# Performance work log

Hardware: AMD Instinct MI355X
Metric: run time of the kernel (lower is better)

## Reference

```python
import jax, jax.numpy as jnp
import numpy as np

B, C, H, W = 4, 128, 128, 128
NUM_OP = 6
LANG_DIM = 256
NHIDDEN = 128
EPS = 1e-5


def setup_inputs() -> dict:
    key = jax.random.key(0)
    ks = jax.random.split(key, 11)
    s = 0.02
    return {
        "x": jax.random.normal(ks[0], (B, C, H, W), jnp.float32),
        "lang_embed": jax.random.normal(ks[1], (B, LANG_DIM), jnp.float32),
        "input_semantics": jax.random.uniform(ks[2], (B, NUM_OP + 2, H, W), jnp.float32),
        # mlp_shared: Linear(lang_dim -> nhidden)
        "Ws": jax.random.normal(ks[3], (NHIDDEN, LANG_DIM), jnp.float32) * s,
        "bs": jnp.zeros((NHIDDEN,), jnp.float32),
        # mlp_gamma / mlp_beta: Linear(nhidden -> num_op)
        "Wg": jax.random.normal(ks[4], (NUM_OP, NHIDDEN), jnp.float32) * s,
        "bg": jnp.zeros((NUM_OP,), jnp.float32),
        "Wb": jax.random.normal(ks[5], (NUM_OP, NHIDDEN), jnp.float32) * s,
        "bb": jnp.zeros((NUM_OP,), jnp.float32),
        # reduce_dim: Linear(num_op -> 1)
        "Wr": jax.random.normal(ks[6], (1, NUM_OP), jnp.float32) * s,
        "br": jnp.zeros((1,), jnp.float32),
    }


def reference(x, lang_embed, input_semantics, Ws, bs, Wg, bg, Wb, bb, Wr, br):
    # InstanceNorm2d(affine=False): computed by the torch module but its result
    # is UNUSED in the num_op>1 branch (dead code in the original; jit will DCE it).
    mean = jnp.mean(x, axis=(2, 3), keepdims=True)
    var = jnp.var(x, axis=(2, 3), keepdims=True)  # biased variance
    _normalized = (x - mean) * jax.lax.rsqrt(var + EPS)

    # Small MLPs on the language embedding (no nonlinearity in the original).
    actv = lang_embed @ Ws.T + bs            # (b, nhidden)
    gamma = actv @ Wg.T + bg                 # (b, num_op)
    beta = actv @ Wb.T + bb                  # (b, num_op)

    sem = jnp.transpose(input_semantics[:, 2:, :, :], (0, 2, 3, 1))  # (b,h,w,num_op)
    g = gamma[:, None, None, :] * sem        # (b,h,w,num_op)
    be = beta[:, None, None, :] * sem        # (b,h,w,num_op)

    # Torch builds out5d = x[...,None]*(1+g)[:,None] + be[:,None]  (b,c,h,w,num_op)
    # then reduce_dim(out5d).squeeze(). Since Linear(num_op->1) is linear, fuse:
    # out = x * (sum_k wr_k + g @ wr) + be @ wr + br  -- identical math, no 5D buffer.
    wr = Wr[0]                               # (num_op,)
    scale = jnp.sum(wr) + jnp.einsum('bhwk,k->bhw', g, wr)   # (b,h,w)
    shift = jnp.einsum('bhwk,k->bhw', be, wr) + br[0]        # (b,h,w)
    out = x * scale[:, None, :, :] + shift[:, None, :, :]    # (b,c,h,w)
    return out
```

## Files before the change

### kernel.cpp

```cpp
#include <hip/hip_runtime.h>

#define HW 16384
#define NCH 128
#define CCH 8
#define LANG 256
#define NH 128
#define NOP 6

typedef float f4 __attribute__((ext_vector_type(4)));

__global__ __launch_bounds__(256) void coef_kernel(
    const float* __restrict__ lang, const float* __restrict__ Ws,
    const float* __restrict__ bs, const float* __restrict__ Wg,
    const float* __restrict__ bg, const float* __restrict__ Wb,
    const float* __restrict__ bb, const float* __restrict__ Wr,
    const float* __restrict__ br, float* __restrict__ coefs) {
  const int b = blockIdx.x;
  const int tid = threadIdx.x;
  const int wave = tid >> 6, lane = tid & 63;
  __shared__ float actv[NH];

  const f4 lv = *(const f4*)(lang + b * LANG + lane * 4);

  #pragma unroll 8
  for (int m = 0; m < 32; ++m) {
    const int j = wave * 32 + m;
    const f4 wv = *(const f4*)(Ws + (size_t)j * LANG + lane * 4);
    float p = lv.x * wv.x + lv.y * wv.y + lv.z * wv.z + lv.w * wv.w;
    #pragma unroll
    for (int off = 32; off; off >>= 1) p += __shfl_xor(p, off);
    if (lane == 0) actv[j] = p + bs[j];
  }
  __syncthreads();

  const float a0 = actv[lane * 2], a1 = actv[lane * 2 + 1];
  #pragma unroll
  for (int r = 0; r < 3; ++r) {
    const int k = wave + 4 * r;
    const int kk = (k < NOP) ? k : k - NOP;
    const float* W = ((k < NOP) ? Wg : Wb) + kk * NH;
    float p = a0 * W[lane * 2] + a1 * W[lane * 2 + 1];
    #pragma unroll
    for (int off = 32; off; off >>= 1) p += __shfl_xor(p, off);
    if (lane == 0) {
      const float bias = (k < NOP) ? bg[kk] : bb[kk];
      coefs[b * 12 + k] = (p + bias) * Wr[kk];
    }
  }
  if (b == 0 && tid == 0) {
    float s = 0.f;
    #pragma unroll
    for (int k = 0; k < NOP; ++k) s += Wr[k];
    coefs[48] = s;
    coefs[49] = br[0];
  }
}

__global__ __launch_bounds__(256) void apply_kernel(
    const float* __restrict__ x, const float* __restrict__ sem,
    const float* __restrict__ coefs, float* __restrict__ out) {
  const int b = blockIdx.z;
  const int cbase = blockIdx.y * CCH;
  const int pix = (blockIdx.x * blockDim.x + threadIdx.x) * 4;

  const float* gk = coefs + b * 12;
  const float wrsum = coefs[48];
  const float brv = coefs[49];

  f4 scale = {wrsum, wrsum, wrsum, wrsum};
  f4 shift = {brv, brv, brv, brv};

  const float* semb = sem + ((size_t)b * 8 + 2) * HW + pix;
  #pragma unroll
  for (int k = 0; k < NOP; ++k) {
    const f4 s = *(const f4*)(semb + (size_t)k * HW);
    const float g = gk[k], be = gk[NOP + k];
    scale += g * s;
    shift += be * s;
  }

  const size_t base = ((size_t)b * NCH + cbase) * HW + pix;
  const float* xb = x + base;
  float* ob = out + base;
  #pragma unroll
  for (int c = 0; c < CCH; ++c) {
    const f4 v = __builtin_nontemporal_load((const f4*)(xb + (size_t)c * HW));
    const f4 r = v * scale + shift;
    __builtin_nontemporal_store(r, (f4*)(ob + (size_t)c * HW));
  }
}

extern "C" void kernel_launch(void* const* d_in, const int* in_sizes, int n_in,
                              void* d_out, int out_size, void* d_ws, size_t ws_size,
                              hipStream_t stream) {
  const float* x    = (const float*)d_in[0];
  const float* lang = (const float*)d_in[1];
  const float* sem  = (const float*)d_in[2];
  const float* Ws   = (const float*)d_in[3];
  const float* bs   = (const float*)d_in[4];
  const float* Wg   = (const float*)d_in[5];
  const float* bg   = (const float*)d_in[6];
  const float* Wb   = (const float*)d_in[7];
  const float* bb   = (const float*)d_in[8];
  const float* Wr   = (const float*)d_in[9];
  const float* br   = (const float*)d_in[10];
  float* out = (float*)d_out;
  float* coefs = (float*)d_ws;

  coef_kernel<<<dim3(4), dim3(256), 0, stream>>>(lang, Ws, bs, Wg, bg, Wb, bb,
                                                 Wr, br, coefs);

  dim3 grid(HW / (256 * 4), NCH / CCH, 4);
  apply_kernel<<<grid, dim3(256), 0, stream>>>(x, sem, coefs, out);
}
```

Measured before the change: 29.15 us.

## Fuse coefficient MLP into apply kernel and double channels per block

Merges the small language-MLP coefficient kernel into the elementwise apply kernel, so every block recomputes the per-batch coefficients in shared memory instead of reading them from a workspace written by a separate launch. Semantic loads are issued before the MLP so their latency overlaps it. Channels per block go from 8 to 16 to amortize the redundant MLP work. Nontemporal loads and stores are replaced with ordinary ones. The aim is to remove a kernel launch and the dependency between the two kernels, at the cost of each block redoing a 256x128 GEMV's worth of weight reads.

```diff
diff --git a/kernel.cpp b/kernel.cpp
--- a/kernel.cpp
+++ b/kernel.cpp
@@ -2,26 +2,36 @@
 
 #define HW 16384
 #define NCH 128
-#define CCH 8
+#define CCH 16
 #define LANG 256
 #define NH 128
 #define NOP 6
 
 typedef float f4 __attribute__((ext_vector_type(4)));
 
-__global__ __launch_bounds__(256) void coef_kernel(
-    const float* __restrict__ lang, const float* __restrict__ Ws,
-    const float* __restrict__ bs, const float* __restrict__ Wg,
-    const float* __restrict__ bg, const float* __restrict__ Wb,
-    const float* __restrict__ bb, const float* __restrict__ Wr,
-    const float* __restrict__ br, float* __restrict__ coefs) {
-  const int b = blockIdx.x;
+__global__ __launch_bounds__(256) void fused_kernel(
+    const float* __restrict__ x, const float* __restrict__ lang,
+    const float* __restrict__ sem,
+    const float* __restrict__ Ws, const float* __restrict__ bs,
+    const float* __restrict__ Wg, const float* __restrict__ bg,
+    const float* __restrict__ Wb, const float* __restrict__ bb,
+    const float* __restrict__ Wr, const float* __restrict__ br,
+    float* __restrict__ out) {
+  const int b = blockIdx.z;
+  const int cbase = blockIdx.y * CCH;
   const int tid = threadIdx.x;
   const int wave = tid >> 6, lane = tid & 63;
+  const int pix = (blockIdx.x * 256 + tid) * 4;
+
   __shared__ float actv[NH];
+  __shared__ float cf[14];
+
+  const float* semb = sem + ((size_t)b * 8 + 2) * HW + pix;
+  f4 sv[NOP];
+  #pragma unroll
+  for (int k = 0; k < NOP; ++k) sv[k] = *(const f4*)(semb + (size_t)k * HW);
 
   const f4 lv = *(const f4*)(lang + b * LANG + lane * 4);
-
   #pragma unroll 8
   for (int m = 0; m < 32; ++m) {
     const int j = wave * 32 + m;
@@ -44,39 +54,25 @@
     for (int off = 32; off; off >>= 1) p += __shfl_xor(p, off);
     if (lane == 0) {
       const float bias = (k < NOP) ? bg[kk] : bb[kk];
-      coefs[b * 12 + k] = (p + bias) * Wr[kk];
+      cf[k] = (p + bias) * Wr[kk];
     }
   }
-  if (b == 0 && tid == 0) {
+  if (tid == 0) {
     float s = 0.f;
     #pragma unroll
     for (int k = 0; k < NOP; ++k) s += Wr[k];
-    coefs[48] = s;
-    coefs[49] = br[0];
+    cf[12] = s;
+    cf[13] = br[0];
   }
-}
+  __syncthreads();
 
-__global__ __launch_bounds__(256) void apply_kernel(
-    const float* __restrict__ x, const float* __restrict__ sem,
-    const float* __restrict__ coefs, float* __restrict__ out) {
-  const int b = blockIdx.z;
-  const int cbase = blockIdx.y * CCH;
-  const int pix = (blockIdx.x * blockDim.x + threadIdx.x) * 4;
-
-  const float* gk = coefs + b * 12;
-  const float wrsum = coefs[48];
-  const float brv = coefs[49];
-
+  const float wrsum = cf[12], brv = cf[13];
   f4 scale = {wrsum, wrsum, wrsum, wrsum};
   f4 shift = {brv, brv, brv, brv};
-
-  const float* semb = sem + ((size_t)b * 8 + 2) * HW + pix;
   #pragma unroll
   for (int k = 0; k < NOP; ++k) {
-    const f4 s = *(const f4*)(semb + (size_t)k * HW);
-    const float g = gk[k], be = gk[NOP + k];
-    scale += g * s;
-    shift += be * s;
+    scale += cf[k] * sv[k];
+    shift += cf[NOP + k] * sv[k];
   }
 
   const size_t base = ((size_t)b * NCH + cbase) * HW + pix;
@@ -84,9 +80,8 @@
   float* ob = out + base;
   #pragma unroll
   for (int c = 0; c < CCH; ++c) {
-    const f4 v = __builtin_nontemporal_load((const f4*)(xb + (size_t)c * HW));
-    const f4 r = v * scale + shift;
-    __builtin_nontemporal_store(r, (f4*)(ob + (size_t)c * HW));
+    const f4 v = *(const f4*)(xb + (size_t)c * HW);
+    *(f4*)(ob + (size_t)c * HW) = v * scale + shift;
   }
 }
 
@@ -105,11 +100,8 @@
   const float* Wr   = (const float*)d_in[9];
   const float* br   = (const float*)d_in[10];
   float* out = (float*)d_out;
-  float* coefs = (float*)d_ws;
-
-  coef_kernel<<<dim3(4), dim3(256), 0, stream>>>(lang, Ws, bs, Wg, bg, Wb, bb,
-                                                 Wr, br, coefs);
 
   dim3 grid(HW / (256 * 4), NCH / CCH, 4);
-  apply_kernel<<<grid, dim3(256), 0, stream>>>(x, sem, coefs, out);
+  fused_kernel<<<grid, dim3(256), 0, stream>>>(x, lang, sem, Ws, bs, Wg, bg,
+                                               Wb, bb, Wr, br, out);
 }
```

Result: slower. 33.88 us (+16.2%).
